# Kernel optimization log

Hardware: AMD Instinct MI355X
Metric: run time of the kernel (lower is better)

## Reference

```python
import jax, jax.numpy as jnp
import numpy as np

B, R, C, D = 8, 64, 16, 128  # batch, num_rows(taxa), patch_num, embed_dim


def _linear_init(key, fan_in, fan_out):
    lim = 1.0 / np.sqrt(fan_in)
    kw, kb = jax.random.split(key)
    W = jax.random.uniform(kw, (fan_in, fan_out), jnp.float32, -lim, lim)
    b = jax.random.uniform(kb, (fan_out,), jnp.float32, -lim, lim)
    return W, b


def setup_inputs() -> dict:
    key = jax.random.key(0)
    ks = jax.random.split(key, 8)
    row_np, col_np = np.triu_indices(R, k=1)  # n = R*(R-1)/2 = 2016 pairs
    hW, hb = _linear_init(ks[1], D, D)
    gW, gb = _linear_init(ks[2], D, D)
    qW, qb = _linear_init(ks[3], D, D)
    kW, kb = _linear_init(ks[4], D, D)
    s1W, s1b = _linear_init(ks[5], D, D)
    s2W, s2b = _linear_init(ks[6], D, 1)
    return {
        "batch_input": jax.random.normal(ks[0], (B, R, C, D), jnp.float32),
        "seq_mask": jnp.ones((B, 1, C), jnp.float32),
        "row": jnp.asarray(row_np, jnp.int32),
        "col": jnp.asarray(col_np, jnp.int32),
        "hW": hW, "hb": hb, "gW": gW, "gb": gb,
        "qW": qW, "qb": qb, "kW": kW, "kb": kb,
        "s1W": s1W, "s1b": s1b, "s2W": s2W, "s2b": s2b,
    }


def reference(batch_input, seq_mask, row, col,
              hW, hb, gW, gb, qW, qb, kW, kb, s1W, s1b, s2W, s2b):
    b, r, c, d = batch_input.shape
    n = row.shape[0]
    # pairwise gather: x_i, x_j -> [b, n, c, d]
    x_i = batch_input[:, row]
    x_j = batch_input[:, col]
    # sigmoid gate fusion of the pair
    h = (x_i - x_j) @ hW + hb
    z = jax.nn.sigmoid(h)
    x = z * x_i + (1.0 - z) * x_j
    # masked global attention over the batch_input 'memory' (r > 2 branch)
    q = x @ qW + qb                    # [b, n, c, d]
    k = batch_input @ kW + kb          # [b, r, c, d]
    scale = 1.0 / np.sqrt(d * c).astype(np.float32)
    alpha = jnp.einsum('bncd,brcd->bnr', q, k) * scale
    # -inf at (pair n, rows row[n] and col[n]); equivalent to += -inf on finite scores
    neg_mask = (jnp.zeros((n, r), bool)
                .at[jnp.arange(n), row].set(True)
                .at[jnp.arange(n), col].set(True))
    alpha = jnp.where(neg_mask[None], -jnp.inf, alpha)
    alpha = jax.nn.softmax(alpha, axis=-1)
    x_glob = jnp.einsum('bnr,brcd->bncd', alpha, batch_input)
    g = x_glob @ gW + gb
    w = jax.nn.sigmoid(g)
    x = (1.0 - w) * x + w * x_glob
    # s_out: Linear -> GELU(exact) -> Linear(d,1), then mask and reduce over c
    s = jax.nn.gelu(x @ s1W + s1b, approximate=False) @ s2W + s2b  # [b, n, c, 1]
    scores = s[..., 0] * seq_mask       # seq_mask [b,1,c] broadcasts over n
    return scores.sum(-1)               # [b, n]
```

## Files before the change

### kernel.cpp

```cpp
#include <hip/hip_runtime.h>
#include <hip/hip_bf16.h>
#include <math.h>

#define B_    8
#define R_    64
#define C_    16
#define D_    128
#define NPAIR 2016
#define CD    2048
#define PG    16
#define NPG   126
#define XSTR  136
#define LSTR  68
#define NEG_BIG (-1e30f)
#define SCALE 0.022097086912079608f

typedef __attribute__((ext_vector_type(8))) short short8;
typedef __attribute__((ext_vector_type(4))) float float4v;

#define WMH  0u
#define WML  16384u
#define WHH  32768u
#define WHL  49152u
#define WGH  65536u
#define WGL  81920u
#define WSH  98304u
#define VECO 131072u
#define QBKO 131592u
#define MO   132616u
#define XTO  1181192u
#define GTO  2229768u
#define HO   3278344u

__device__ __forceinline__ unsigned short f2b(float f){
    union { float f; unsigned int u; } v; v.f = f;
    const unsigned int r = v.u + 0x7FFFu + ((v.u >> 16) & 1u);
    return (unsigned short)(r >> 16);
}
__device__ __forceinline__ float b2f(unsigned short u){
    union { unsigned int i; float f; } v; v.i = ((unsigned int)u) << 16; return v.f;
}
__device__ __forceinline__ float lo2f(unsigned int u){
    union { unsigned int i; float f; } v; v.i = u << 16; return v.f;
}
__device__ __forceinline__ float hif2f(unsigned int u){
    union { unsigned int i; float f; } v; v.i = u & 0xffff0000u; return v.f;
}
__device__ __forceinline__ unsigned int pack2(float a, float b){
    unsigned int r;
    asm("v_cvt_pk_bf16_f32 %0, %1, %2" : "=v"(r) : "v"(a), "v"(b));
    return r;
}
__device__ __forceinline__ unsigned short f2b1(float a){
    unsigned int r;
    asm("v_cvt_pk_bf16_f32 %0, %1, %1" : "=v"(r) : "v"(a));
    return (unsigned short)r;
}
__device__ __forceinline__ void split_bf(float v, float* hi, float* lo){
    union { float f; unsigned int u; } x; x.f = v;
    const unsigned int r = (x.u + 0x7FFFu + ((x.u >> 16) & 1u)) & 0xffff0000u;
    union { unsigned int u; float f; } h; h.u = r;
    *hi = h.f; *lo = v - h.f;
}
__device__ __forceinline__ float sigmoid_safe(float x){
    return __builtin_amdgcn_rcpf(1.f + __expf(-x));
}
__device__ __forceinline__ float gelu_tanh(float x){
    const float u = x*x;
    const float g2 = x*(1.5957691216057308f + 0.07135481627159f*u);
    return x * sigmoid_safe(g2);
}

__global__ __launch_bounds__(256) void k_prepA(
    const float* __restrict__ x,
    const float* __restrict__ hW, const float* __restrict__ gW,
    const float* __restrict__ qW, const float* __restrict__ qb,
    const float* __restrict__ kW, const float* __restrict__ kb,
    unsigned short* __restrict__ ws)
{
    __shared__ __align__(16) unsigned short tile[128*69];
    const int bid = blockIdx.x, t = threadIdx.x;
    if (bid < 64){
        __shared__ float sKW[2][128];
        const int e0 = bid*2;
        sKW[t>>7][t&127] = kW[(e0 + (t>>7))*128 + (t&127)];
        __syncthreads();
        const int e = t>>7, d = t&127;
        const float* qr = qW + d*128;
        const float* kr = sKW[e];
        float acc = 0.f;
        #pragma unroll 8
        for (int g = 0; g < 128; g += 4){
            const float4 qv = *reinterpret_cast<const float4*>(qr + g);
            acc += qv.x*kr[g] + qv.y*kr[g+1] + qv.z*kr[g+2] + qv.w*kr[g+3];
        }
        float hi, lo; split_bf(acc, &hi, &lo);
        ws[WMH + d*128 + (e0+e)] = f2b(hi);
        ws[WML + d*128 + (e0+e)] = f2b(lo);
    } else if (bid == 64){
        float* vec = (float*)(ws + VECO);
        if (t < 128){
            float a1 = 0.f, a2 = 0.f;
            #pragma unroll 8
            for (int g = 0; g < 128; g += 4){
                const float4 q4 = *reinterpret_cast<const float4*>(qW + t*128 + g);
                const float4 k4 = *reinterpret_cast<const float4*>(kW + t*128 + g);
                const float4 kb4 = *reinterpret_cast<const float4*>(kb + g);
                const float4 qb4 = *reinterpret_cast<const float4*>(qb + g);
                a1 += q4.x*kb4.x + q4.y*kb4.y + q4.z*kb4.z + q4.w*kb4.w;
                a2 += k4.x*qb4.x + k4.y*qb4.y + k4.z*qb4.z + k4.w*qb4.w;
            }
            vec[t] = a1;
            vec[128 + t] = a2;
        } else if (t == 128){
            float a = 0.f;
            for (int g = 0; g < 128; ++g) a = fmaf(qb[g], kb[g], a);
            vec[256] = a;
        }
    } else if (bid < 193){
        const int j = bid - 65;
        const int mat = j >> 6;
        const int gid = (j & 63)*256 + t;
        const int n = gid >> 7, k = gid & 127;
        const float* W = (mat==0) ? hW : gW;
        const unsigned int baseh = (mat==0) ? WHH : WGH;
        const unsigned int basel = (mat==0) ? WHL : WGL;
        float hi, lo; split_bf(W[k*128 + n], &hi, &lo);
        ws[baseh + gid] = f2b(hi);
        ws[basel + gid] = f2b(lo);
    } else {
        const int blk = bid - 193;
        const int b = blk >> 4, cd0 = (blk & 15)*128;
        #pragma unroll
        for (int i = 0; i < 32; ++i){
            const int idx = i*256 + t;
            const int r = idx >> 7, cc = idx & 127;
            tile[cc*69 + r] = f2b(x[((size_t)(b*64 + r))*CD + cd0 + cc]);
        }
        __syncthreads();
        const unsigned int base = XTO + (unsigned int)(b*2048 + cd0)*64;
        #pragma unroll
        for (int j = 0; j < 32; ++j){
            const int idx = j*256 + t;
            const int cc = idx >> 6, r = idx & 63;
            ws[base + cc*64 + r] = tile[cc*69 + r];
        }
    }
}

__global__ __launch_bounds__(512) void k_prepB(const float* __restrict__ x,
        const float* __restrict__ gb, const float* __restrict__ s1W,
        unsigned short* __restrict__ ws)
{
    __shared__ __align__(16) unsigned short smem[8832];
    __shared__ float sQ[4];
    const int bid = blockIdx.x, t = threadIdx.x;
    const int w = t >> 6, lane = t & 63, l15 = lane & 15, quad = lane >> 4;

    if (bid < 256){
        const bool isM = (bid >= 128);
        unsigned short* sH = smem;
        const int br0 = (bid & 127) * 4;
        const float* kqf = (const float*)(ws + VECO) + 128;
        const float* mbf = (const float*)(ws + VECO);
        if (t < 4) sQ[t] = 0.f;
        __syncthreads();
        float qacc[4] = {0.f, 0.f, 0.f, 0.f};
        #pragma unroll
        for (int i = 0; i < 4; ++i){
            const int flat = (t + 512*i)*4;
            const int lr = i;
            const int cd = flat & 2047;
            const float4 v = *reinterpret_cast<const float4*>(x + (size_t)(br0+lr)*CD + cd);
            const int ad = (lr*16 + (cd>>7))*XSTR + lr*8 + (cd & 127);
            uint2 uh;
            uh.x = pack2(v.x, v.y); uh.y = pack2(v.z, v.w);
            *reinterpret_cast<uint2*>(sH + ad) = uh;
            if (isM){
                const float4 kq4 = *reinterpret_cast<const float4*>(kqf + (cd & 127));
                qacc[i] = v.x*kq4.x + v.y*kq4.y + v.z*kq4.z + v.w*kq4.w;
            }
        }
        if (isM){
            #pragma unroll
            for (int i = 0; i < 4; ++i){
                float s = qacc[i];
                #pragma unroll
                for (int off = 1; off < 64; off <<= 1) s += __shfl_xor(s, off);
                if (lane == 0) atomicAdd(&sQ[i], s);
            }
        }
        __syncthreads();
        const unsigned short* Bh = isM ? (ws+WMH) : (ws+WHH);
        const unsigned short* Bl = isM ? (ws+WML) : (ws+WHL);
        const float bv = isM ? mbf[w*16 + l15] : 0.f;
        float4v acc[4];
        #pragma unroll
        for (int mt = 0; mt < 4; ++mt){ float4v d = {bv,bv,bv,bv}; acc[mt] = d; }
        #pragma unroll
        for (int ks = 0; ks < 4; ++ks){
            const int ko = ks*32 + quad*8;
            const int bd = (w*16 + l15)*128 + ko;
            const short8 bh = *reinterpret_cast<const short8*>(Bh + bd);
            const short8 bl = *reinterpret_cast<const short8*>(Bl + bd);
            #pragma unroll
            for (int mt = 0; mt < 4; ++mt){
                const int ad = (mt*16 + l15)*XSTR + mt*8 + ko;
                const short8 ah = *reinterpret_cast<const short8*>(sH + ad);
                float4v d = acc[mt];
                d = __builtin_amdgcn_mfma_f32_16x16x32_bf16(ah, bh, d, 0,0,0);
                d = __builtin_amdgcn_mfma_f32_16x16x32_bf16(ah, bl, d, 0,0,0);
                acc[mt] = d;
            }
        }
        const int f = w*16 + l15;
        const unsigned int dsto = isM ? MO : HO;
        #pragma unroll
        for (int mt = 0; mt < 4; ++mt)
        #pragma unroll
        for (int e = 0; e < 4; ++e){
            const int c = quad*4 + e;
            ws[dsto + (size_t)(br0+mt)*CD + c*128 + f] = f2b(acc[mt][e]);
        }
        if (isM && t < 4){
            const float s0 = ((const float*)(ws + VECO))[256];
            ((float*)(ws + QBKO))[br0 + t] = sQ[t] + 16.f*s0;
        }
    } else if (bid < 384){
        unsigned short* tileB = smem;
        const int gidx = bid - 256;
        const int b = gidx >> 4, cd0 = (gidx & 15)*128;
        #pragma unroll
        for (int i = 0; i < 16; ++i){
            const int idx = i*512 + t;
            const int r = idx >> 7, dd = idx & 127;
            tileB[r*138 + dd] = f2b(x[(size_t)(b*64 + r)*CD + cd0 + dd]);
        }
        __syncthreads();
        float4v acc[4];
        #pragma unroll
        for (int nt = 0; nt < 4; ++nt){ float4v z = {0.f,0.f,0.f,0.f}; acc[nt] = z; }
        #pragma unroll
        for (int ks = 0; ks < 4; ++ks){
            const int ko = ks*32 + quad*8;
            const int adg = (w*16 + l15)*128 + ko;
            const short8 ah = *reinterpret_cast<const short8*>(ws + WGH + adg);
            const short8 al = *reinterpret_cast<const short8*>(ws + WGL + adg);
            #pragma unroll
            for (int nt = 0; nt < 4; ++nt){
                const short8 bb = *reinterpret_cast<const short8*>(tileB + (nt*16 + l15)*138 + ko);
                float4v d = acc[nt];
                d = __builtin_amdgcn_mfma_f32_16x16x32_bf16(ah, bb, d, 0,0,0);
                d = __builtin_amdgcn_mfma_f32_16x16x32_bf16(al, bb, d, 0,0,0);
                acc[nt] = d;
            }
        }
        #pragma unroll
        for (int nt = 0; nt < 4; ++nt)
        #pragma unroll
        for (int e = 0; e < 4; ++e){
            const int f = w*16 + quad*4 + e;
            const float val = acc[nt][e] + gb[f];
            ws[GTO + (size_t)(b*2048 + cd0 + f)*64 + nt*16 + l15] = f2b(val);
        }
    } else {
        const int gid = (bid - 384)*4096 + t;
        #pragma unroll
        for (int i = 0; i < 8; ++i){
            const int g = gid + i*512;
            const int n = g >> 7, k = g & 127;
            ws[WSH + g] = f2b(s1W[k*128 + n]);
        }
    }
}

__global__ __launch_bounds__(512, 4) void k_main(
    const float* __restrict__ x, const float* __restrict__ seq_mask,
    const int* __restrict__ row, const int* __restrict__ col,
    const float* __restrict__ hb, const float* __restrict__ s1b,
    const float* __restrict__ s2W, const float* __restrict__ s2b,
    const unsigned short* __restrict__ ws, float* __restrict__ out)
{
    __shared__ __align__(16) unsigned short sX[256*XSTR + 128];
    __shared__ __align__(16) unsigned short sAl[16*72];
    __shared__ float sLog[16*LSTR];
    __shared__ float sOut[PG];
    __shared__ float sMask[16];
    __shared__ int srp[PG], scp[PG];

    const int t = threadIdx.x;
    const int w = t >> 6, lane = t & 63, l15 = lane & 15, quad = lane >> 4;
    const int b = blockIdx.x, p0 = blockIdx.y * PG;
    const float* xb = x + (size_t)b * R_ * CD;
    const unsigned short* Hb = ws + HO + (size_t)b * R_ * CD;

    if (t < PG){ srp[t] = row[p0+t]; scp[t] = col[p0+t]; sOut[t] = 0.f; }
    if (t >= 32 && t < 48) sMask[t-32] = seq_mask[b*C_ + (t-32)];
    for (int i = t; i < 1152; i += 512) sAl[i] = 0;
    for (int i = t; i < 16*LSTR; i += 512) sLog[i] = 0.f;
    __syncthreads();

    #pragma unroll 4
    for (int i = 0; i < 16; ++i){
        const int flat = (t + 512*i)*4;
        const int p = flat >> 11, cd = flat & 2047;
        const int ri = srp[p], ci = scp[p];
        const float4 xi = *reinterpret_cast<const float4*>(xb + (size_t)ri*CD + cd);
        const float4 xj = *reinterpret_cast<const float4*>(xb + (size_t)ci*CD + cd);
        const uint2 Hi2 = *reinterpret_cast<const uint2*>(Hb + (size_t)ri*CD + cd);
        const uint2 Hj2 = *reinterpret_cast<const uint2*>(Hb + (size_t)ci*CD + cd);
        const float4 h4 = *reinterpret_cast<const float4*>(hb + (cd & 127));
        const float z0 = sigmoid_safe(lo2f(Hi2.x)  - lo2f(Hj2.x)  + h4.x);
        const float z1 = sigmoid_safe(hif2f(Hi2.x) - hif2f(Hj2.x) + h4.y);
        const float z2 = sigmoid_safe(lo2f(Hi2.y)  - lo2f(Hj2.y)  + h4.z);
        const float z3 = sigmoid_safe(hif2f(Hi2.y) - hif2f(Hj2.y) + h4.w);
        const float v0 = xj.x + z0*(xi.x - xj.x);
        const float v1 = xj.y + z1*(xi.y - xj.y);
        const float v2 = xj.z + z2*(xi.z - xj.z);
        const float v3 = xj.w + z3*(xi.w - xj.w);
        const int ad = (p*16 + (cd>>7))*XSTR + p*8 + (cd & 127);
        uint2 uv; uv.x = pack2(v0,v1); uv.y = pack2(v2,v3);
        *reinterpret_cast<uint2*>(sX + ad) = uv;
    }
    __syncthreads();

    {
        const int rt = w & 3, kh = w >> 2;
        const int r = rt*16 + l15;
        const unsigned short* Mr = ws + MO + ((size_t)b*64 + r)*CD + kh*1024;
        float4v d = {0.f,0.f,0.f,0.f};
        #pragma unroll 8
        for (int ks = 0; ks < 32; ++ks){
            const int k = kh*1024 + ks*32 + quad*8;
            const short8 ah = *reinterpret_cast<const short8*>(
                sX + (l15*16 + (k>>7))*XSTR + l15*8 + (k & 127));
            const short8 bh = *reinterpret_cast<const short8*>(Mr + ks*32 + quad*8);
            d = __builtin_amdgcn_mfma_f32_16x16x32_bf16(ah, bh, d, 0,0,0);
        }
        #pragma unroll
        for (int e = 0; e < 4; ++e){
            const int pp = quad*4 + e;
            atomicAdd(&sLog[pp*LSTR + r], d[e]);
        }
    }
    __syncthreads();

    if (t < 256){
        const int pp = t >> 4, l = t & 15;
        const int ri = srp[pp], ci = scp[pp];
        const float* qbk = (const float*)(ws + QBKO);
        float v[4]; float m = NEG_BIG;
        #pragma unroll
        for (int k = 0; k < 4; ++k){
            const int r = l + 16*k;
            float lv = (sLog[pp*LSTR + r] + qbk[b*64 + r]) * SCALE;
            if (r == ri || r == ci) lv = NEG_BIG;
            v[k] = lv; m = fmaxf(m, lv);
        }
        #pragma unroll
        for (int s = 1; s < 16; s <<= 1) m = fmaxf(m, __shfl_xor(m, s));
        float e4[4]; float sum = 0.f;
        #pragma unroll
        for (int k = 0; k < 4; ++k){
            const int r = l + 16*k;
            const bool masked = (r == ri || r == ci);
            const float e = masked ? 0.f : __expf(fmaxf(v[k]-m, -80.f));
            e4[k] = e; sum += e;
        }
        #pragma unroll
        for (int s = 1; s < 16; s <<= 1) sum += __shfl_xor(sum, s);
        const float inv = __builtin_amdgcn_rcpf(sum);
        #pragma unroll
        for (int k = 0; k < 4; ++k) sAl[pp*72 + l + 16*k] = f2b1(e4[k]*inv);
    }
    __syncthreads();

    {
        const unsigned short* XTb = ws + XTO + (size_t)b * CD * 64;
        const unsigned short* GTb = ws + GTO + (size_t)b * CD * 64;
        const short8 Ah0 = *reinterpret_cast<const short8*>(sAl + l15*72 + quad*8);
        const short8 Ah1 = *reinterpret_cast<const short8*>(sAl + l15*72 + 32 + quad*8);
        #pragma unroll 4
        for (int j = 0; j < 16; ++j){
            const int cd = w*256 + j*16 + l15;
            const short8 xb0 = *reinterpret_cast<const short8*>(XTb + (size_t)cd*64 + quad*8);
            const short8 xb1 = *reinterpret_cast<const short8*>(XTb + (size_t)cd*64 + 32 + quad*8);
            const short8 gb0 = *reinterpret_cast<const short8*>(GTb + (size_t)cd*64 + quad*8);
            const short8 gb1 = *reinterpret_cast<const short8*>(GTb + (size_t)cd*64 + 32 + quad*8);
            float4v dx = {0.f,0.f,0.f,0.f}, dg = {0.f,0.f,0.f,0.f};
            dx = __builtin_amdgcn_mfma_f32_16x16x32_bf16(Ah0, xb0, dx, 0,0,0);
            dx = __builtin_amdgcn_mfma_f32_16x16x32_bf16(Ah1, xb1, dx, 0,0,0);
            dg = __builtin_amdgcn_mfma_f32_16x16x32_bf16(Ah0, gb0, dg, 0,0,0);
            dg = __builtin_amdgcn_mfma_f32_16x16x32_bf16(Ah1, gb1, dg, 0,0,0);
            #pragma unroll
            for (int e = 0; e < 4; ++e){
                const int pp = quad*4 + e;
                const int ad = (pp*16 + (cd>>7))*XSTR + pp*8 + (cd & 127);
                const float wv = sigmoid_safe(dg[e]);
                const float xo = b2f(sX[ad]);
                sX[ad] = f2b1((1.f - wv)*xo + wv*dx[e]);
            }
        }
    }
    __syncthreads();

    {
        float4v acc16[16];
        const float bv = s1b[w*16 + l15];
        #pragma unroll
        for (int mt = 0; mt < 16; ++mt){ float4v d = {bv,bv,bv,bv}; acc16[mt] = d; }
        #pragma unroll
        for (int ks = 0; ks < 4; ++ks){
            const int ko = ks*32 + quad*8;
            const int bd = (w*16 + l15)*128 + ko;
            const short8 bh = *reinterpret_cast<const short8*>(ws + WSH + bd);
            #pragma unroll
            for (int mt = 0; mt < 16; ++mt){
                const short8 a = *reinterpret_cast<const short8*>(sX + (mt*16 + l15)*XSTR + mt*8 + ko);
                acc16[mt] = __builtin_amdgcn_mfma_f32_16x16x32_bf16(a, bh, acc16[mt], 0,0,0);
            }
        }
        const float s2v = s2W[w*16 + l15];
        const float mk0 = sMask[quad*4+0], mk1 = sMask[quad*4+1];
        const float mk2 = sMask[quad*4+2], mk3 = sMask[quad*4+3];
        float psum[16];
        #pragma unroll
        for (int mt = 0; mt < 16; ++mt){
            float s = gelu_tanh(acc16[mt][0]) * mk0;
            s += gelu_tanh(acc16[mt][1]) * mk1;
            s += gelu_tanh(acc16[mt][2]) * mk2;
            s += gelu_tanh(acc16[mt][3]) * mk3;
            psum[mt] = s * s2v;
        }
        #pragma unroll
        for (int s = 1; s < 64; s <<= 1)
            #pragma unroll
            for (int mt = 0; mt < 16; ++mt) psum[mt] += __shfl_xor(psum[mt], s);
        if (lane == 0){
            #pragma unroll
            for (int mt = 0; mt < 16; ++mt) atomicAdd(&sOut[mt], psum[mt]);
        }
    }
    __syncthreads();

    if (t < PG){
        float msum = 0.f;
        #pragma unroll
        for (int c = 0; c < 16; ++c) msum += sMask[c];
        out[(size_t)b*NPAIR + p0 + t] = sOut[t] + s2b[0]*msum;
    }
}

extern "C" void kernel_launch(void* const* d_in, const int* in_sizes, int n_in,
                              void* d_out, int out_size, void* d_ws, size_t ws_size,
                              hipStream_t stream)
{
    const float* x    = (const float*)d_in[0];
    const float* mask = (const float*)d_in[1];
    const int*   row  = (const int*)d_in[2];
    const int*   col  = (const int*)d_in[3];
    const float* hW  = (const float*)d_in[4];  const float* hb  = (const float*)d_in[5];
    const float* gW  = (const float*)d_in[6];  const float* gb  = (const float*)d_in[7];
    const float* qW  = (const float*)d_in[8];  const float* qb  = (const float*)d_in[9];
    const float* kW  = (const float*)d_in[10]; const float* kb  = (const float*)d_in[11];
    const float* s1W = (const float*)d_in[12]; const float* s1b = (const float*)d_in[13];
    const float* s2W = (const float*)d_in[14]; const float* s2b = (const float*)d_in[15];

    unsigned short* ws = (unsigned short*)d_ws;

    k_prepA<<<321, 256, 0, stream>>>(x, hW, gW, qW, qb, kW, kb, ws);
    k_prepB<<<388, 512, 0, stream>>>(x, gb, s1W, ws);
    k_main<<<dim3(B_, NPG), 512, 0, stream>>>(x, mask, row, col,
                                              hb, s1b, s2W, s2b,
                                              ws, (float*)d_out);
}
```

Before: 228.5 us.

## Halve pairs per block to raise occupancy and split MFMA accumulator chains

Reduces the pair-group size per block from 16 to 8, doubling the grid and halving LDS and accumulator register use so more blocks can be resident (launch bounds raised to 6). The logits MFMA loop now uses four independent accumulators to break the serial dependency chain. Because the MFMA tile is still 16 rows, half the rows are duplicates and their outputs are discarded, so MFMA work and weight re-reads per pair roughly double.

```diff
diff --git a/kernel.cpp b/kernel.cpp
--- a/kernel.cpp
+++ b/kernel.cpp
@@ -8,8 +8,8 @@
 #define D_    128
 #define NPAIR 2016
 #define CD    2048
-#define PG    16
-#define NPG   126
+#define PG    8
+#define NPG   252
 #define XSTR  136
 #define LSTR  68
 #define NEG_BIG (-1e30f)
@@ -274,16 +274,16 @@
     }
 }
 
-__global__ __launch_bounds__(512, 4) void k_main(
+__global__ __launch_bounds__(512, 6) void k_main(
     const float* __restrict__ x, const float* __restrict__ seq_mask,
     const int* __restrict__ row, const int* __restrict__ col,
     const float* __restrict__ hb, const float* __restrict__ s1b,
     const float* __restrict__ s2W, const float* __restrict__ s2b,
     const unsigned short* __restrict__ ws, float* __restrict__ out)
 {
-    __shared__ __align__(16) unsigned short sX[256*XSTR + 128];
-    __shared__ __align__(16) unsigned short sAl[16*72];
-    __shared__ float sLog[16*LSTR];
+    __shared__ __align__(16) unsigned short sX[128*XSTR + 128];
+    __shared__ __align__(16) unsigned short sAl[8*72];
+    __shared__ float sLog[8*LSTR];
     __shared__ float sOut[PG];
     __shared__ float sMask[16];
     __shared__ int srp[PG], scp[PG];
@@ -296,12 +296,12 @@
 
     if (t < PG){ srp[t] = row[p0+t]; scp[t] = col[p0+t]; sOut[t] = 0.f; }
     if (t >= 32 && t < 48) sMask[t-32] = seq_mask[b*C_ + (t-32)];
-    for (int i = t; i < 1152; i += 512) sAl[i] = 0;
-    for (int i = t; i < 16*LSTR; i += 512) sLog[i] = 0.f;
+    for (int i = t; i < 8*72; i += 512) sAl[i] = 0;
+    for (int i = t; i < 8*LSTR; i += 512) sLog[i] = 0.f;
     __syncthreads();
 
     #pragma unroll 4
-    for (int i = 0; i < 16; ++i){
+    for (int i = 0; i < 8; ++i){
         const int flat = (t + 512*i)*4;
         const int p = flat >> 11, cd = flat & 2047;
         const int ri = srp[p], ci = scp[p];
@@ -327,25 +327,36 @@
     {
         const int rt = w & 3, kh = w >> 2;
         const int r = rt*16 + l15;
+        const int pr = l15 & 7;
         const unsigned short* Mr = ws + MO + ((size_t)b*64 + r)*CD + kh*1024;
-        float4v d = {0.f,0.f,0.f,0.f};
-        #pragma unroll 8
-        for (int ks = 0; ks < 32; ++ks){
-            const int k = kh*1024 + ks*32 + quad*8;
-            const short8 ah = *reinterpret_cast<const short8*>(
-                sX + (l15*16 + (k>>7))*XSTR + l15*8 + (k & 127));
-            const short8 bh = *reinterpret_cast<const short8*>(Mr + ks*32 + quad*8);
-            d = __builtin_amdgcn_mfma_f32_16x16x32_bf16(ah, bh, d, 0,0,0);
-        }
-        #pragma unroll
-        for (int e = 0; e < 4; ++e){
-            const int pp = quad*4 + e;
-            atomicAdd(&sLog[pp*LSTR + r], d[e]);
-        }
-    }
-    __syncthreads();
-
-    if (t < 256){
+        float4v d0 = {0.f,0.f,0.f,0.f}, d1 = {0.f,0.f,0.f,0.f};
+        float4v d2 = {0.f,0.f,0.f,0.f}, d3 = {0.f,0.f,0.f,0.f};
+        #pragma unroll
+        for (int ks = 0; ks < 32; ks += 4){
+            #pragma unroll
+            for (int u = 0; u < 4; ++u){
+                const int k = kh*1024 + (ks+u)*32 + quad*8;
+                const short8 ah = *reinterpret_cast<const short8*>(
+                    sX + (pr*16 + (k>>7))*XSTR + pr*8 + (k & 127));
+                const short8 bh = *reinterpret_cast<const short8*>(Mr + (ks+u)*32 + quad*8);
+                if (u == 0) d0 = __builtin_amdgcn_mfma_f32_16x16x32_bf16(ah, bh, d0, 0,0,0);
+                else if (u == 1) d1 = __builtin_amdgcn_mfma_f32_16x16x32_bf16(ah, bh, d1, 0,0,0);
+                else if (u == 2) d2 = __builtin_amdgcn_mfma_f32_16x16x32_bf16(ah, bh, d2, 0,0,0);
+                else d3 = __builtin_amdgcn_mfma_f32_16x16x32_bf16(ah, bh, d3, 0,0,0);
+            }
+        }
+        const float4v d = (d0 + d1) + (d2 + d3);
+        if (quad < 2){
+            #pragma unroll
+            for (int e = 0; e < 4; ++e){
+                const int pp = quad*4 + e;
+                atomicAdd(&sLog[pp*LSTR + r], d[e]);
+            }
+        }
+    }
+    __syncthreads();
+
+    if (t < 128){
         const int pp = t >> 4, l = t & 15;
         const int ri = srp[pp], ci = scp[pp];
         const float* qbk = (const float*)(ws + QBKO);
@@ -378,8 +389,9 @@
     {
         const unsigned short* XTb = ws + XTO + (size_t)b * CD * 64;
         const unsigned short* GTb = ws + GTO + (size_t)b * CD * 64;
-        const short8 Ah0 = *reinterpret_cast<const short8*>(sAl + l15*72 + quad*8);
-        const short8 Ah1 = *reinterpret_cast<const short8*>(sAl + l15*72 + 32 + quad*8);
+        const int pr = l15 & 7;
+        const short8 Ah0 = *reinterpret_cast<const short8*>(sAl + pr*72 + quad*8);
+        const short8 Ah1 = *reinterpret_cast<const short8*>(sAl + pr*72 + 32 + quad*8);
         #pragma unroll 4
         for (int j = 0; j < 16; ++j){
             const int cd = w*256 + j*16 + l15;
@@ -392,53 +404,55 @@
             dx = __builtin_amdgcn_mfma_f32_16x16x32_bf16(Ah1, xb1, dx, 0,0,0);
             dg = __builtin_amdgcn_mfma_f32_16x16x32_bf16(Ah0, gb0, dg, 0,0,0);
             dg = __builtin_amdgcn_mfma_f32_16x16x32_bf16(Ah1, gb1, dg, 0,0,0);
-            #pragma unroll
-            for (int e = 0; e < 4; ++e){
-                const int pp = quad*4 + e;
-                const int ad = (pp*16 + (cd>>7))*XSTR + pp*8 + (cd & 127);
-                const float wv = sigmoid_safe(dg[e]);
-                const float xo = b2f(sX[ad]);
-                sX[ad] = f2b1((1.f - wv)*xo + wv*dx[e]);
+            if (quad < 2){
+                #pragma unroll
+                for (int e = 0; e < 4; ++e){
+                    const int pp = quad*4 + e;
+                    const int ad = (pp*16 + (cd>>7))*XSTR + pp*8 + (cd & 127);
+                    const float wv = sigmoid_safe(dg[e]);
+                    const float xo = b2f(sX[ad]);
+                    sX[ad] = f2b1((1.f - wv)*xo + wv*dx[e]);
+                }
             }
         }
     }
     __syncthreads();
 
     {
-        float4v acc16[16];
+        float4v acc8[8];
         const float bv = s1b[w*16 + l15];
         #pragma unroll
-        for (int mt = 0; mt < 16; ++mt){ float4v d = {bv,bv,bv,bv}; acc16[mt] = d; }
+        for (int mt = 0; mt < 8; ++mt){ float4v d = {bv,bv,bv,bv}; acc8[mt] = d; }
         #pragma unroll
         for (int ks = 0; ks < 4; ++ks){
             const int ko = ks*32 + quad*8;
             const int bd = (w*16 + l15)*128 + ko;
             const short8 bh = *reinterpret_cast<const short8*>(ws + WSH + bd);
             #pragma unroll
-            for (int mt = 0; mt < 16; ++mt){
+            for (int mt = 0; mt < 8; ++mt){
                 const short8 a = *reinterpret_cast<const short8*>(sX + (mt*16 + l15)*XSTR + mt*8 + ko);
-                acc16[mt] = __builtin_amdgcn_mfma_f32_16x16x32_bf16(a, bh, acc16[mt], 0,0,0);
+                acc8[mt] = __builtin_amdgcn_mfma_f32_16x16x32_bf16(a, bh, acc8[mt], 0,0,0);
             }
         }
         const float s2v = s2W[w*16 + l15];
         const float mk0 = sMask[quad*4+0], mk1 = sMask[quad*4+1];
         const float mk2 = sMask[quad*4+2], mk3 = sMask[quad*4+3];
-        float psum[16];
-        #pragma unroll
-        for (int mt = 0; mt < 16; ++mt){
-            float s = gelu_tanh(acc16[mt][0]) * mk0;
-            s += gelu_tanh(acc16[mt][1]) * mk1;
-            s += gelu_tanh(acc16[mt][2]) * mk2;
-            s += gelu_tanh(acc16[mt][3]) * mk3;
+        float psum[8];
+        #pragma unroll
+        for (int mt = 0; mt < 8; ++mt){
+            float s = gelu_tanh(acc8[mt][0]) * mk0;
+        s += gelu_tanh(acc8[mt][1]) * mk1;
+            s += gelu_tanh(acc8[mt][2]) * mk2;
+            s += gelu_tanh(acc8[mt][3]) * mk3;
             psum[mt] = s * s2v;
         }
         #pragma unroll
         for (int s = 1; s < 64; s <<= 1)
             #pragma unroll
-            for (int mt = 0; mt < 16; ++mt) psum[mt] += __shfl_xor(psum[mt], s);
+            for (int mt = 0; mt < 8; ++mt) psum[mt] += __shfl_xor(psum[mt], s);
         if (lane == 0){
             #pragma unroll
-            for (int mt = 0; mt < 16; ++mt) atomicAdd(&sOut[mt], psum[mt]);
+            for (int mt = 0; mt < 8; ++mt) atomicAdd(&sOut[mt], psum[mt]);
         }
     }
     __syncthreads();
```

New measurement: 299.3 us. 31.0% more time.
